# Kernel optimization log

Hardware: AMD Instinct MI355X
Metric: run time of the kernel (lower is better)

## Reference

```python
import jax, jax.numpy as jnp
import numpy as np

B, T, E, H, D = 4, 2048, 1024, 16, 64  # batch, seq (==context), embed, heads, head_size


def setup_inputs() -> dict:
    key = jax.random.key(0)
    ks = jax.random.split(key, 5)
    s_in = 1.0 / np.sqrt(E)
    s_c = 1.0 / np.sqrt(H * D)
    return {
        "x": jax.random.normal(ks[0], (B, T, E), dtype=jnp.float32),
        "Wq": jax.random.normal(ks[1], (H, E, D), dtype=jnp.float32) * s_in,
        "Wk": jax.random.normal(ks[2], (H, E, D), dtype=jnp.float32) * s_in,
        "Wv": jax.random.normal(ks[3], (H, E, D), dtype=jnp.float32) * s_in,
        "Wc": jax.random.normal(ks[4], (H * D, E), dtype=jnp.float32) * s_c,
    }


def reference(x, Wq, Wk, Wv, Wc):
    # Batched equivalent of the per-head Python loop: each head h does
    # q = x @ Wq[h], k = x @ Wk[h], v = x @ Wv[h]; causal softmax attention.
    q = jnp.einsum("bse,hed->bhsd", x, Wq)
    k = jnp.einsum("bte,hed->bhtd", x, Wk)
    v = jnp.einsum("bte,hed->bhtd", x, Wv)
    scale = 1.0 / jnp.sqrt(jnp.asarray(D, dtype=x.dtype))
    scores = jnp.einsum("bhsd,bhtd->bhst", q, k) * scale  # [B,H,T,T]
    causal = jnp.tril(jnp.ones((T, T), dtype=bool))
    scores = jnp.where(causal[None, None], scores, jnp.asarray(-jnp.inf, dtype=scores.dtype))
    attn = jax.nn.softmax(scores, axis=-1)
    out = jnp.einsum("bhst,bhtd->bhsd", attn, v)
    # concat heads along last dim (head 0 first), then combine linear
    out = out.transpose(0, 2, 1, 3).reshape(B, T, H * D)
    return out @ Wc
```

## Files before the change

### kernel.cpp

```cpp
#include <hip/hip_runtime.h>
#include <cstdint>
#include <cstddef>

typedef unsigned short u16;
typedef __bf16 bf16x8 __attribute__((ext_vector_type(8)));
typedef float f32x4 __attribute__((ext_vector_type(4)));
typedef float f32x16 __attribute__((ext_vector_type(16)));

#define B_ 4
#define T_ 2048
#define E_ 1024
#define H_ 16
#define D_ 64
#define HD3_ 3072
#define M_ (B_*T_)

#if __has_builtin(__builtin_amdgcn_exp2f)
#define EXP2F(x) __builtin_amdgcn_exp2f(x)
#else
#define EXP2F(x) exp2f(x)
#endif
#if __has_builtin(__builtin_amdgcn_rcpf)
#define RCPF(x) __builtin_amdgcn_rcpf(x)
#else
#define RCPF(x) (1.f/(x))
#endif

__device__ __forceinline__ u16 f2bf(float f) {
  union { float f; unsigned u; } v; v.f = f;
  unsigned r = v.u + 0x7FFFu + ((v.u >> 16) & 1u);
  return (u16)(r >> 16);
}

__device__ __forceinline__ unsigned cvtpk(float a, float b) {
  unsigned r;
  asm("v_cvt_pk_bf16_f32 %0, %1, %2" : "=v"(r) : "v"(a), "v"(b));
  return r;
}

__device__ __forceinline__ void gl2lds16(const u16* g, u16* l) {
  __builtin_amdgcn_global_load_lds(
      (const __attribute__((address_space(1))) unsigned int*)g,
      (__attribute__((address_space(3))) unsigned int*)l, 16, 0, 0);
}

__global__ void prep_x(const float* __restrict__ x, u16* __restrict__ xb) {
  const long n4 = (long)(M_) * E_ / 4;
  for (long i = (long)blockIdx.x * blockDim.x + threadIdx.x; i < n4;
       i += (long)gridDim.x * blockDim.x) {
    float4 v = ((const float4*)x)[i];
    unsigned lo = (unsigned)f2bf(v.x) | ((unsigned)f2bf(v.y) << 16);
    unsigned hi = (unsigned)f2bf(v.z) | ((unsigned)f2bf(v.w) << 16);
    ((uint2*)xb)[i] = make_uint2(lo, hi);
  }
}

__global__ __launch_bounds__(256) void prep_w(
    const float* __restrict__ Wq, const float* __restrict__ Wk,
    const float* __restrict__ Wv, const float* __restrict__ Wc,
    u16* __restrict__ WT, u16* __restrict__ WcT, float qscale)
{
  __shared__ u16 tile[64][72];
  const int id = blockIdx.x;
  const int tid = threadIdx.x, lane = tid & 63;
  const float* src; int srcStride; u16* dst; float scale = 1.f;
  if (id < 768) {
    int mtxh = id >> 4, et = id & 15;
    int mtx = mtxh >> 4, h = mtxh & 15;
    const float* W = (mtx == 0) ? Wq : (mtx == 1) ? Wk : Wv;
    src = W + (size_t)h * 65536 + (size_t)(et * 64) * 64;
    srcStride = 64;
    dst = WT + (size_t)(mtx * 1024 + h * 64) * 1024 + et * 64;
    if (mtx == 0) scale = qscale;
  } else {
    int j = id - 768;
    int kt = j >> 4, nt = j & 15;
    src = Wc + (size_t)(kt * 64) * 1024 + nt * 64;
    srcStride = 1024;
    dst = WcT + (size_t)(nt * 64) * 1024 + kt * 64;
  }
#pragma unroll
  for (int i = 0; i < 4; ++i) {
    int u = i * 256 + tid, r = u >> 4, c4 = (u & 15) * 4;
    float4 v = *(const float4*)(src + (size_t)r * srcStride + c4);
    *(uint2*)&tile[r][c4] = make_uint2(
        (unsigned)f2bf(v.x * scale) | ((unsigned)f2bf(v.y * scale) << 16),
        (unsigned)f2bf(v.z * scale) | ((unsigned)f2bf(v.w * scale) << 16));
  }
  __syncthreads();
#pragma unroll
  for (int i = 0; i < 2; ++i) {
    int grp = i * 4 + (tid >> 6);
    u16 tmp[8];
#pragma unroll
    for (int j = 0; j < 8; ++j) tmp[j] = tile[grp * 8 + j][lane];
    *(uint4*)(dst + (size_t)lane * 1024 + grp * 8) = *(uint4*)tmp;
  }
}

template<int N_, bool OUT_BF16>
__global__ __launch_bounds__(512, 2) void gemm8(
    const u16* __restrict__ A, const u16* __restrict__ Bt, void* __restrict__ Cv)
{
  __shared__ u16 As[2][128 * 64];
  __shared__ u16 Bs[2][256 * 64];
  const int tid = threadIdx.x;
  const int lane = tid & 63, w = tid >> 6;
  const int wr = w >> 2, wc = w & 3;
  const int l15 = lane & 15, l4 = lane >> 4;

  const int gx = N_ / 256;
  const int lin = blockIdx.x;
  const int cpx = (gx * 64) >> 3;
  const int swz = (lin & 7) * cpx + (lin >> 3);
  const int bxi = swz % gx, byi = swz / gx;
  const size_t bm = (size_t)byi * 128, bn = (size_t)bxi * 256;
  const u16* Ag = A + bm * 1024;
  const u16* Bg = Bt + bn * 1024;

  auto stageA = [&](int b, int t, int i) {
    int idx = i * 512 + tid, r = idx >> 3, c = idx & 7;
    gl2lds16(Ag + (size_t)r * 1024 + t * 64 + ((c ^ (r & 7)) * 8), &As[b][idx * 8]);
  };
  auto stageB = [&](int b, int t, int i) {
    int idx = i * 512 + tid, r = idx >> 3, c = idx & 7;
    gl2lds16(Bg + (size_t)r * 1024 + t * 64 + ((c ^ (r & 7)) * 8), &Bs[b][idx * 8]);
  };

  int aoff[4][2], boff[4][2];
#pragma unroll
  for (int m = 0; m < 4; ++m) {
    int r = wr * 64 + m * 16 + l15;
#pragma unroll
    for (int s = 0; s < 2; ++s)
      aoff[m][s] = r * 64 + (((s * 4 + l4) ^ (r & 7)) * 8);
  }
#pragma unroll
  for (int n = 0; n < 4; ++n) {
    int r = wc * 64 + n * 16 + l15;
#pragma unroll
    for (int s = 0; s < 2; ++s)
      boff[n][s] = r * 64 + (((s * 4 + l4) ^ (r & 7)) * 8);
  }

  f32x4 acc[4][4] = {};

#pragma unroll
  for (int i = 0; i < 2; ++i) stageA(0, 0, i);
#pragma unroll
  for (int i = 0; i < 4; ++i) stageB(0, 0, i);
#pragma unroll
  for (int i = 0; i < 2; ++i) stageA(1, 1, i);
  asm volatile("s_waitcnt vmcnt(2)" ::: "memory");
  __builtin_amdgcn_s_barrier();

  for (int t = 0; t < 16; ++t) {
    const int cur = t & 1;
    bf16x8 af[4][2], bfv[4][2];
#pragma unroll
    for (int m = 0; m < 4; ++m)
#pragma unroll
      for (int s = 0; s < 2; ++s)
        af[m][s] = *(const bf16x8*)&As[cur][aoff[m][s]];
#pragma unroll
    for (int n = 0; n < 2; ++n)
#pragma unroll
      for (int s = 0; s < 2; ++s)
        bfv[n][s] = *(const bf16x8*)&Bs[cur][boff[n][s]];
    if (t + 1 < 16) {
      stageB(cur ^ 1, t + 1, 0);
      stageB(cur ^ 1, t + 1, 1);
      stageB(cur ^ 1, t + 1, 2);
    }
    __builtin_amdgcn_s_barrier();
    asm volatile("s_waitcnt lgkmcnt(0)" ::: "memory");
    __builtin_amdgcn_sched_barrier(0);
    __builtin_amdgcn_s_setprio(1);
#pragma unroll
    for (int m = 0; m < 4; ++m)
#pragma unroll
      for (int n = 0; n < 2; ++n)
#pragma unroll
        for (int s = 0; s < 2; ++s)
          acc[m][n] = __builtin_amdgcn_mfma_f32_16x16x32_bf16(
              af[m][s], bfv[n][s], acc[m][n], 0, 0, 0);
    __builtin_amdgcn_s_setprio(0);
    __builtin_amdgcn_s_barrier();

#pragma unroll
    for (int n = 2; n < 4; ++n)
#pragma unroll
      for (int s = 0; s < 2; ++s)
        bfv[n][s] = *(const bf16x8*)&Bs[cur][boff[n][s]];
    if (t + 1 < 16) stageB(cur ^ 1, t + 1, 3);
    if (t + 2 < 16) { stageA(cur, t + 2, 0); stageA(cur, t + 2, 1); }
    __builtin_amdgcn_s_barrier();
    asm volatile("s_waitcnt lgkmcnt(0)" ::: "memory");
    __builtin_amdgcn_sched_barrier(0);
    __builtin_amdgcn_s_setprio(1);
#pragma unroll
    for (int m = 0; m < 4; ++m)
#pragma unroll
      for (int n = 2; n < 4; ++n)
#pragma unroll
        for (int s = 0; s < 2; ++s)
          acc[m][n] = __builtin_amdgcn_mfma_f32_16x16x32_bf16(
              af[m][s], bfv[n][s], acc[m][n], 0, 0, 0);
    __builtin_amdgcn_s_setprio(0);
    if (t + 2 < 16)      asm volatile("s_waitcnt vmcnt(2)" ::: "memory");
    else if (t + 1 < 16) asm volatile("s_waitcnt vmcnt(0)" ::: "memory");
    __builtin_amdgcn_s_barrier();
  }

#pragma unroll
  for (int m = 0; m < 4; ++m)
#pragma unroll
    for (int n = 0; n < 4; ++n) {
      size_t row = bm + wr * 64 + m * 16 + l4 * 4;
      size_t col = bn + wc * 64 + n * 16 + l15;
#pragma unroll
      for (int j = 0; j < 4; ++j) {
        if (OUT_BF16)
          ((u16*)Cv)[(row + j) * N_ + col] = f2bf(acc[m][n][j]);
        else
          ((float*)Cv)[(row + j) * N_ + col] = acc[m][n][j];
      }
    }
}

__global__ __launch_bounds__(256) void transpose_v(const u16* __restrict__ QKV,
                                                   u16* __restrict__ VT) {
  const int bh = blockIdx.y, b = bh >> 4, h = bh & 15;
  const int t0 = blockIdx.x * 64;
  __shared__ u16 tile[64][72];
  const int tid = threadIdx.x, lane = tid & 63;
  const u16* src = QKV + ((size_t)(b * T_ + t0) * HD3_ + 2048 + h * 64);
#pragma unroll
  for (int i = 0; i < 2; ++i) {
    int c = i * 256 + tid, r = c >> 3, cc = (c & 7) * 8;
    *(uint4*)&tile[r][cc] = *(const uint4*)(src + (size_t)r * HD3_ + cc);
  }
  __syncthreads();
  u16* dst = VT + (size_t)bh * (D_ * T_) + t0;
#pragma unroll
  for (int i = 0; i < 2; ++i) {
    int grp = i * 4 + (tid >> 6);
    u16 tmp[8];
#pragma unroll
    for (int j = 0; j < 8; ++j) tmp[j] = tile[grp * 8 + j][lane];
    *(uint4*)(dst + (size_t)lane * T_ + grp * 8) = *(uint4*)tmp;
  }
}

__global__ __launch_bounds__(256, 4) void attn_kernel(
    const u16* __restrict__ QKV, const u16* __restrict__ VT,
    u16* __restrict__ O)
{
  __shared__ u16 Ks[2][4096];
  __shared__ u16 Vs[2][4096];
  const int L = blockIdx.x;
  const int bh = L & 63, b = bh >> 4, h = bh & 15;
  const int jj = L >> 8, gg = (L >> 6) & 3;
  const int qt = 4 * jj + ((gg + jj) & 3);
  const int q0 = qt * 128;
  const int tid = threadIdx.x, w = tid >> 6, lane = tid & 63;
  const int ql = lane & 31, hi = lane >> 5;
  const int qw0 = q0 + w * 32;

  const u16* Qg = QKV + ((size_t)(b * T_ + q0) * HD3_ + h * 64);
  const u16* Kg = QKV + ((size_t)(b * T_) * HD3_ + 1024 + h * 64);
  const u16* Vg = VT + (size_t)bh * (D_ * T_);

#pragma unroll
  for (int i = 0; i < 4; ++i) {
    int c = i * 256 + tid, r = c >> 3, cc = c & 7, sc = cc ^ (r & 7);
    gl2lds16(Qg + (size_t)r * HD3_ + sc * 8, &Ks[0][0] + c * 8);
  }
  __syncthreads();
  bf16x8 qf[4];
  {
    int qrow = w * 32 + ql;
#pragma unroll
    for (int s = 0; s < 4; ++s) {
      int ch = (2 * s + hi) ^ (qrow & 7);
      qf[s] = *(const bf16x8*)(&Ks[0][0] + qrow * 64 + ch * 8);
    }
  }
  __syncthreads();

  int koff[2][4];
#pragma unroll
  for (int f = 0; f < 2; ++f) {
    int row = f * 32 + ql, swzr = row & 7;
#pragma unroll
    for (int s = 0; s < 4; ++s)
      koff[f][s] = row * 64 + (((2 * s + hi) ^ swzr) * 8);
  }

  const int c0 = tid, c1 = 256 + tid;
  const int r0_ = c0 >> 3, sc0 = (c0 & 7) ^ (r0_ & 7);
  const int r1_ = c1 >> 3, sc1 = (c1 & 7) ^ (r1_ & 7);
  const int lo0 = c0 * 8, lo1 = c1 * 8;
  const u16* kp0 = Kg + (size_t)r0_ * HD3_ + sc0 * 8;
  const u16* kp1 = Kg + (size_t)r1_ * HD3_ + sc1 * 8;
  const u16* vp0 = Vg + (size_t)r0_ * T_ + sc0 * 8;
  const u16* vp1 = Vg + (size_t)r1_ * T_ + sc1 * 8;

  gl2lds16(kp0, &Ks[0][lo0]);
  gl2lds16(kp1, &Ks[0][lo1]);
  gl2lds16(vp0, &Vs[0][lo0]);
  gl2lds16(vp1, &Vs[0][lo1]);
  kp0 += 64 * HD3_; kp1 += 64 * HD3_;
  vp0 += 64; vp1 += 64;

  f32x16 acc[2];
#pragma unroll
  for (int ni = 0; ni < 2; ++ni)
#pragma unroll
    for (int r = 0; r < 16; ++r) acc[ni][r] = 0.f;
  float mrun = -1e30f, lrun = 0.f;
  const int ktmax = 2 * qt + 2;

  for (int kt = 0; kt < ktmax; ++kt) {
    const int cur = kt & 1;
    const int kv0 = kt * 64;
    __syncthreads();
    if (kt + 1 < ktmax) {
      u16* kb = &Ks[cur ^ 1][0];
      u16* vb = &Vs[cur ^ 1][0];
      gl2lds16(kp0, kb + lo0);
      gl2lds16(kp1, kb + lo1);
      gl2lds16(vp0, vb + lo0);
      gl2lds16(vp1, vb + lo1);
      kp0 += 64 * HD3_; kp1 += 64 * HD3_;
      vp0 += 64; vp1 += 64;
    }
    if (kv0 > qw0 + 31) continue;
    const u16* kbase = &Ks[cur][0];
    const u16* vbase = &Vs[cur][0];

    f32x16 st[2];
#pragma unroll
    for (int f = 0; f < 2; ++f)
#pragma unroll
      for (int r = 0; r < 16; ++r) st[f][r] = 0.f;
    __builtin_amdgcn_s_setprio(1);
#pragma unroll
    for (int f = 0; f < 2; ++f)
#pragma unroll
      for (int s = 0; s < 4; ++s) {
        bf16x8 kfr = *(const bf16x8*)(kbase + koff[f][s]);
        st[f] = __builtin_amdgcn_mfma_f32_32x32x16_bf16(kfr, qf[s], st[f], 0, 0, 0);
      }
    __builtin_amdgcn_s_setprio(0);

    if (kv0 + 63 > qw0) {
      const int qg = qw0 + ql;
#pragma unroll
      for (int f = 0; f < 2; ++f)
#pragma unroll
        for (int r = 0; r < 16; ++r) {
          int kg = kv0 + f * 32 + (r & 3) + 8 * (r >> 2) + 4 * hi;
          if (kg > qg) st[f][r] = -1e30f;
        }
    }

    float tr[16];
#pragma unroll
    for (int r = 0; r < 16; ++r) tr[r] = fmaxf(st[0][r], st[1][r]);
#pragma unroll
    for (int ss = 8; ss; ss >>= 1)
#pragma unroll
      for (int r = 0; r < 8; ++r)
        if (r < ss) tr[r] = fmaxf(tr[r], tr[r + ss]);
    float mt = fmaxf(tr[0], __shfl_xor(tr[0], 32, 64));
    if (!__all(mt - mrun <= 8.f)) {
      float mnew = fmaxf(mrun, mt);
      float corr = EXP2F(mrun - mnew);
      lrun *= corr;
#pragma unroll
      for (int ni = 0; ni < 2; ++ni)
#pragma unroll
        for (int r = 0; r < 16; ++r) acc[ni][r] *= corr;
      mrun = mnew;
    }
#pragma unroll
    for (int f = 0; f < 2; ++f)
#pragma unroll
      for (int r = 0; r < 16; ++r) st[f][r] = EXP2F(st[f][r] - mrun);
#pragma unroll
    for (int r = 0; r < 16; ++r) tr[r] = st[0][r] + st[1][r];
#pragma unroll
    for (int ss = 8; ss; ss >>= 1)
#pragma unroll
      for (int r = 0; r < 8; ++r)
        if (r < ss) tr[r] += tr[r + ss];
    lrun += tr[0] + __shfl_xor(tr[0], 32, 64);

    __builtin_amdgcn_s_setprio(1);
#pragma unroll
    for (int s = 0; s < 4; ++s) {
      const int f = s >> 1, bse = (s & 1) * 8;
      unsigned b0 = cvtpk(st[f][bse + 0], st[f][bse + 1]);
      unsigned b1 = cvtpk(st[f][bse + 2], st[f][bse + 3]);
      unsigned a0 = cvtpk(st[f][bse + 4], st[f][bse + 5]);
      unsigned a1 = cvtpk(st[f][bse + 6], st[f][bse + 7]);
      asm volatile("v_permlane32_swap_b32 %0, %1" : "+v"(b0), "+v"(a0));
      asm volatile("v_permlane32_swap_b32 %0, %1" : "+v"(b1), "+v"(a1));
      union { unsigned u[4]; bf16x8 v; } pa;
      pa.u[0] = b0; pa.u[1] = b1; pa.u[2] = a0; pa.u[3] = a1;
#pragma unroll
      for (int ni = 0; ni < 2; ++ni) {
        bf16x8 vf = *(const bf16x8*)(vbase + koff[ni][s]);
        acc[ni] = __builtin_amdgcn_mfma_f32_32x32x16_bf16(vf, pa.v, acc[ni], 0, 0, 0);
      }
    }
    __builtin_amdgcn_s_setprio(0);
  }

  const int q = q0 + w * 32 + ql;
  u16* Og = O + ((size_t)(b * T_ + q) * (H_ * D_) + h * 64);
  const float inv = RCPF(lrun);
#pragma unroll
  for (int ni = 0; ni < 2; ++ni)
#pragma unroll
    for (int rr = 0; rr < 8; ++rr) {
      const int r0 = rr * 2;
      const int d0 = ((r0 & 3) + 8 * (r0 >> 2)) + 4 * hi + ni * 32;
      unsigned pk = cvtpk(acc[ni][r0] * inv, acc[ni][r0 + 1] * inv);
      *(unsigned*)(Og + d0) = pk;
    }
}

extern "C" void kernel_launch(void* const* d_in, const int* in_sizes, int n_in,
                              void* d_out, int out_size, void* d_ws, size_t ws_size,
                              hipStream_t stream) {
  const float* x  = (const float*)d_in[0];
  const float* Wq = (const float*)d_in[1];
  const float* Wk = (const float*)d_in[2];
  const float* Wv = (const float*)d_in[3];
  const float* Wc = (const float*)d_in[4];

  char* ws = (char*)d_ws;
  u16* xb  = (u16*)(ws);
  u16* WT  = (u16*)(ws + 16777216);
  u16* WcT = (u16*)(ws + 23068672);
  u16* QKV = (u16*)(ws + 25165824);
  u16* Ob  = (u16*)(ws + 75497472);
  u16* VT  = xb;
  float* out = (float*)d_out;

  const float QSCALE = 0.125f * 1.4426950408889634f;

  prep_x<<<2048, 256, 0, stream>>>(x, xb);
  prep_w<<<1024, 256, 0, stream>>>(Wq, Wk, Wv, Wc, WT, WcT, QSCALE);
  gemm8<3072, true><<<768, 512, 0, stream>>>(xb, WT, QKV);
  transpose_v<<<dim3(32, 64), 256, 0, stream>>>(QKV, VT);
  attn_kernel<<<dim3(1024), 256, 0, stream>>>(QKV, VT, Ob);
  gemm8<1024, false><<<256, 512, 0, stream>>>(Ob, WcT, out);
}
```

Measured before the change: 253.3 us.

## Triple-buffer GEMM LDS staging with single barrier per K-step

Replaces the double-buffered, split-half GEMM main loop with a three-stage LDS ring that prefetches two K-steps ahead. Each iteration then needs only one barrier and one full MFMA block instead of two half-phases with three barriers. The aim is to hide global-to-LDS latency better and cut synchronisation. In exchange, LDS use grows by half, which likely prevents two blocks per CU, and more B fragments are held in registers at once.

```diff
diff --git a/kernel.cpp b/kernel.cpp
--- a/kernel.cpp
+++ b/kernel.cpp
@@ -99,11 +99,11 @@
 }
 
 template<int N_, bool OUT_BF16>
-__global__ __launch_bounds__(512, 2) void gemm8(
+__global__ __launch_bounds__(512, 2) void gemm3(
     const u16* __restrict__ A, const u16* __restrict__ Bt, void* __restrict__ Cv)
 {
-  __shared__ u16 As[2][128 * 64];
-  __shared__ u16 Bs[2][256 * 64];
+  __shared__ u16 As[3][128 * 64];
+  __shared__ u16 Bs[3][256 * 64];
   const int tid = threadIdx.x;
   const int lane = tid & 63, w = tid >> 6;
   const int wr = w >> 2, wc = w & 3;
@@ -118,13 +118,19 @@
   const u16* Ag = A + bm * 1024;
   const u16* Bg = Bt + bn * 1024;
 
-  auto stageA = [&](int b, int t, int i) {
-    int idx = i * 512 + tid, r = idx >> 3, c = idx & 7;
-    gl2lds16(Ag + (size_t)r * 1024 + t * 64 + ((c ^ (r & 7)) * 8), &As[b][idx * 8]);
+  auto stageA = [&](int b, int t) {
+#pragma unroll
+    for (int i = 0; i < 2; ++i) {
+      int idx = i * 512 + tid, r = idx >> 3, c = idx & 7;
+      gl2lds16(Ag + (size_t)r * 1024 + t * 64 + ((c ^ (r & 7)) * 8), &As[b][idx * 8]);
+    }
   };
-  auto stageB = [&](int b, int t, int i) {
-    int idx = i * 512 + tid, r = idx >> 3, c = idx & 7;
-    gl2lds16(Bg + (size_t)r * 1024 + t * 64 + ((c ^ (r & 7)) * 8), &Bs[b][idx * 8]);
+  auto stageB = [&](int b, int t) {
+#pragma unroll
+    for (int i = 0; i < 4; ++i) {
+      int idx = i * 512 + tid, r = idx >> 3, c = idx & 7;
+      gl2lds16(Bg + (size_t)r * 1024 + t * 64 + ((c ^ (r & 7)) * 8), &Bs[b][idx * 8]);
+    }
   };
 
   int aoff[4][2], boff[4][2];
@@ -145,17 +151,18 @@
 
   f32x4 acc[4][4] = {};
 
-#pragma unroll
-  for (int i = 0; i < 2; ++i) stageA(0, 0, i);
-#pragma unroll
-  for (int i = 0; i < 4; ++i) stageB(0, 0, i);
-#pragma unroll
-  for (int i = 0; i < 2; ++i) stageA(1, 1, i);
-  asm volatile("s_waitcnt vmcnt(2)" ::: "memory");
+  stageA(0, 0); stageB(0, 0);
+  stageA(1, 1); stageB(1, 1);
+  asm volatile("s_waitcnt vmcnt(6)" ::: "memory");
+  __builtin_amdgcn_sched_barrier(0);
   __builtin_amdgcn_s_barrier();
-
+  __builtin_amdgcn_sched_barrier(0);
+
+  int cur = 0;
   for (int t = 0; t < 16; ++t) {
-    const int cur = t & 1;
+    const int sb = (cur >= 1) ? cur - 1 : 2;
+    if (t + 2 < 16) { stageA(sb, t + 2); stageB(sb, t + 2); }
+
     bf16x8 af[4][2], bfv[4][2];
 #pragma unroll
     for (int m = 0; m < 4; ++m)
@@ -163,53 +170,29 @@
       for (int s = 0; s < 2; ++s)
         af[m][s] = *(const bf16x8*)&As[cur][aoff[m][s]];
 #pragma unroll
-    for (int n = 0; n < 2; ++n)
+    for (int n = 0; n < 4; ++n)
 #pragma unroll
       for (int s = 0; s < 2; ++s)
         bfv[n][s] = *(const bf16x8*)&Bs[cur][boff[n][s]];
-    if (t + 1 < 16) {
-      stageB(cur ^ 1, t + 1, 0);
-      stageB(cur ^ 1, t + 1, 1);
-      stageB(cur ^ 1, t + 1, 2);
-    }
-    __builtin_amdgcn_s_barrier();
-    asm volatile("s_waitcnt lgkmcnt(0)" ::: "memory");
-    __builtin_amdgcn_sched_barrier(0);
+
     __builtin_amdgcn_s_setprio(1);
 #pragma unroll
     for (int m = 0; m < 4; ++m)
 #pragma unroll
-      for (int n = 0; n < 2; ++n)
+      for (int n = 0; n < 4; ++n)
 #pragma unroll
         for (int s = 0; s < 2; ++s)
           acc[m][n] = __builtin_amdgcn_mfma_f32_16x16x32_bf16(
               af[m][s], bfv[n][s], acc[m][n], 0, 0, 0);
     __builtin_amdgcn_s_setprio(0);
+
+    asm volatile("s_waitcnt lgkmcnt(0)" ::: "memory");
+    if (t + 2 < 16)      asm volatile("s_waitcnt vmcnt(6)" ::: "memory");
+    else if (t == 14)    asm volatile("s_waitcnt vmcnt(0)" ::: "memory");
+    __builtin_amdgcn_sched_barrier(0);
     __builtin_amdgcn_s_barrier();
-
-#pragma unroll
-    for (int n = 2; n < 4; ++n)
-#pragma unroll
-      for (int s = 0; s < 2; ++s)
-        bfv[n][s] = *(const bf16x8*)&Bs[cur][boff[n][s]];
-    if (t + 1 < 16) stageB(cur ^ 1, t + 1, 3);
-    if (t + 2 < 16) { stageA(cur, t + 2, 0); stageA(cur, t + 2, 1); }
-    __builtin_amdgcn_s_barrier();
-    asm volatile("s_waitcnt lgkmcnt(0)" ::: "memory");
     __builtin_amdgcn_sched_barrier(0);
-    __builtin_amdgcn_s_setprio(1);
-#pragma unroll
-    for (int m = 0; m < 4; ++m)
-#pragma unroll
-      for (int n = 2; n < 4; ++n)
-#pragma unroll
-        for (int s = 0; s < 2; ++s)
-          acc[m][n] = __builtin_amdgcn_mfma_f32_16x16x32_bf16(
-              af[m][s], bfv[n][s], acc[m][n], 0, 0, 0);
-    __builtin_amdgcn_s_setprio(0);
-    if (t + 2 < 16)      asm volatile("s_waitcnt vmcnt(2)" ::: "memory");
-    else if (t + 1 < 16) asm volatile("s_waitcnt vmcnt(0)" ::: "memory");
-    __builtin_amdgcn_s_barrier();
+    cur = (cur >= 2) ? 0 : cur + 1;
   }
 
 #pragma unroll
@@ -454,8 +437,8 @@
 
   prep_x<<<2048, 256, 0, stream>>>(x, xb);
   prep_w<<<1024, 256, 0, stream>>>(Wq, Wk, Wv, Wc, WT, WcT, QSCALE);
-  gemm8<3072, true><<<768, 512, 0, stream>>>(xb, WT, QKV);
+  gemm3<3072, true><<<768, 512, 0, stream>>>(xb, WT, QKV);
   transpose_v<<<dim3(32, 64), 256, 0, stream>>>(QKV, VT);
   attn_kernel<<<dim3(1024), 256, 0, stream>>>(QKV, VT, Ob);
-  gemm8<1024, false><<<256, 512, 0, stream>>>(Ob, WcT, out);
-}
+  gemm3<1024, false><<<256, 512, 0, stream>>>(Ob, WcT, out);
+}
```

New measurement: 268.7 us. +6.1%, slower.
